# Kernel tuning notes

Hardware: AMD Instinct MI355X
Metric: run time of the kernel (lower is better)

The kernel has to match this reference:

```python
import jax, jax.numpy as jnp
import numpy as np

R_MAX = 32
S_MAX = 2
C_Z = 128
C_REL = 4 * R_MAX + 2 * S_MAX + 7 - 2 * R_MAX - 2 + 42  # 115
C_TOK = C_REL - (2 * R_MAX + 2) - (2 * S_MAX + 2) - 1    # 42


def setup_inputs() -> dict:
    key = jax.random.key(0)
    k0, k1, k2, k3, k4, k5 = jax.random.split(key, 6)
    B, N = 1, 1024
    asym_id = jax.random.randint(k0, (B, N), 0, 8)
    sym_id = jax.random.randint(k1, (B, N), 0, 8)
    entity_id = jax.random.randint(k2, (B, N), 0, 4)
    residue_index = jnp.sort(jax.random.randint(k3, (B, N), 0, 600), axis=-1)
    rel_tok_feat = jax.random.uniform(k4, (B, N, N, C_TOK), dtype=jnp.float32)
    W = jax.random.normal(k5, (C_REL, C_Z), dtype=jnp.float32) * 0.02
    return {
        "rel_tok_feat": rel_tok_feat,
        "W": W,
        "asym_id": asym_id,
        "sym_id": sym_id,
        "entity_id": entity_id,
        "residue_index": residue_index,
    }


def reference(rel_tok_feat, W, asym_id, sym_id, entity_id, residue_index):
    dt = rel_tok_feat.dtype
    # pairwise comparisons: [B, N, N]
    chain_same = asym_id[..., None] == asym_id[..., None, :]
    entity_same = entity_id[..., None] == entity_id[..., None, :]

    # relative residue offset, clipped, out-of-chain -> bin 2*r_max+1
    residue_offset = residue_index[..., None] - residue_index[..., None, :] + R_MAX
    clipped_res = jnp.clip(residue_offset, 0, 2 * R_MAX)
    d_res = jnp.where(chain_same, clipped_res, 2 * R_MAX + 1)
    rel_pos_feat = jax.nn.one_hot(d_res, 2 * R_MAX + 2, dtype=dt)  # [B,N,N,66]

    # relative chain offset
    chain_offset = sym_id[..., None] - sym_id[..., None, :] + S_MAX
    clipped_chain = jnp.clip(chain_offset, 0, 2 * S_MAX)
    d_chain = jnp.where(chain_same | (~entity_same), 2 * S_MAX + 1, clipped_chain)
    rel_chain_feat = jax.nn.one_hot(d_chain, 2 * S_MAX + 2, dtype=dt)  # [B,N,N,6]

    rel_feat = jnp.concatenate(
        [rel_pos_feat, rel_tok_feat, entity_same[..., None].astype(dt), rel_chain_feat],
        axis=-1,
    )  # [B,N,N,115]
    # Linear(c_rel_feat -> c_z, bias=False)
    return jnp.einsum("bijf,fc->bijc", rel_feat, W)
```

## Files before the change

kernel.cpp:

```cpp
#include <hip/hip_runtime.h>


typedef __attribute__((ext_vector_type(8))) short short8;
typedef __attribute__((ext_vector_type(4))) float floatx4;

#define NSEQ    1024
#define NTOK    42
#define CZ      128
#define CHUNK   64
#define NCHUNK  8
#define THREADS 256
#define TOK_DW  21
#define LDS_AW  36
#define NGROWS  73

__device__ __forceinline__ unsigned short f2bf(float f) {
    union { float f; unsigned int i; } v; v.f = f;
    unsigned int i = v.i;
    return (unsigned short)((i + 0x7fffu + ((i >> 16) & 1u)) >> 16);
}
__device__ __forceinline__ unsigned int packbf2(float x, float y) {
    return ((unsigned int)f2bf(y) << 16) | (unsigned int)f2bf(x);
}

__global__ __launch_bounds__(THREADS) void relpos_kernel(
    const float* __restrict__ tok,
    const float* __restrict__ W,
    const int* __restrict__ asym,
    const int* __restrict__ sym,
    const int* __restrict__ eid,
    const int* __restrict__ res,
    float* __restrict__ out)
{
    __shared__ __align__(16) unsigned int lds_Au[CHUNK * LDS_AW];
    __shared__ float lds_W[NGROWS * CZ];
    __shared__ int lds_flags[CHUNK];

    const int tid  = threadIdx.x;
    const int lane = tid & 63;
    const int wv   = tid >> 6;
    const int n    = lane & 15;
    const int q    = lane >> 4;

    for (int u = tid; u < NGROWS * CZ; u += THREADS) {
        int row = u >> 7;
        int wrow = row + (row >= 66 ? 42 : 0);
        lds_W[u] = W[wrow * CZ + (u & 127)];
    }

    short8 bfrag[2][8];
    #pragma unroll
    for (int ks = 0; ks < 2; ++ks) {
        #pragma unroll
        for (int nt = 0; nt < 8; ++nt) {
            short8 b;
            #pragma unroll
            for (int j = 0; j < 8; ++j) {
                int k = ks * 32 + q * 8 + j;
                b[j] = (k < NTOK) ? (short)f2bf(W[(66 + k) * CZ + nt * 16 + n]) : (short)0;
            }
            bfrag[ks][nt] = b;
        }
    }

    const int pblock = blockIdx.x * (CHUNK * NCHUNK);

    for (int ch = 0; ch < NCHUNK; ++ch) {
        const int p0 = pblock + ch * CHUNK;
        __syncthreads();

        const float2* tokv = (const float2*)tok + (size_t)p0 * TOK_DW;
        for (int u = tid; u < CHUNK * TOK_DW; u += THREADS) {
            float2 d = tokv[u];
            int pr = u / TOK_DW;
            int cu = u - pr * TOK_DW;
            lds_Au[pr * LDS_AW + cu] = packbf2(d.x, d.y);
        }
        for (int u = tid; u < CHUNK * 11; u += THREADS) {
            int pr = u / 11;
            lds_Au[pr * LDS_AW + 21 + (u - pr * 11)] = 0;
        }
        if (tid < CHUNK) {
            int p = p0 + tid;
            int i = p >> 10, j = p & (NSEQ - 1);
            bool cs = asym[i] == asym[j];
            bool es = eid[i] == eid[j];
            int ro = res[i] - res[j] + 32;
            ro = ro < 0 ? 0 : (ro > 64 ? 64 : ro);
            int dres = cs ? ro : 65;
            int co = sym[i] - sym[j] + 2;
            co = co < 0 ? 0 : (co > 4 ? 4 : co);
            int dch = (cs || !es) ? 5 : co;
            lds_flags[tid] = dres | (dch << 8) | ((es ? 1 : 0) << 16);
        }
        __syncthreads();

        const unsigned short* arow = (const unsigned short*)&lds_Au[(wv * 16 + n) * LDS_AW];
        short8 a0 = *(const short8*)(arow + q * 8);
        short8 a1 = *(const short8*)(arow + 32 + q * 8);
        floatx4 acc[8];
        #pragma unroll
        for (int nt = 0; nt < 8; ++nt) {
            floatx4 z = {0.f, 0.f, 0.f, 0.f};
            z = __builtin_amdgcn_mfma_f32_16x16x32_bf16(a0, bfrag[0][nt], z, 0, 0, 0);
            z = __builtin_amdgcn_mfma_f32_16x16x32_bf16(a1, bfrag[1][nt], z, 0, 0, 0);
            acc[nt] = z;
        }

        #pragma unroll
        for (int r = 0; r < 4; ++r) {
            int pl = wv * 16 + q * 4 + r;
            int fl = lds_flags[pl];
            const float* wres = lds_W + (fl & 0xff) * CZ;
            const float* wch  = lds_W + (67 + ((fl >> 8) & 0xff)) * CZ;
            float entf = (fl >> 16) ? 1.0f : 0.0f;
            const float* went = lds_W + 66 * CZ;
            size_t obase = ((size_t)(p0 + pl)) * CZ;
            #pragma unroll
            for (int nt = 0; nt < 8; ++nt) {
                int c = nt * 16 + n;
                out[obase + c] = acc[nt][r] + wres[c] + entf * went[c] + wch[c];
            }
        }
    }
}

extern "C" void kernel_launch(void* const* d_in, const int* in_sizes, int n_in,
                              void* d_out, int out_size, void* d_ws, size_t ws_size,
                              hipStream_t stream) {
    const float* tok = (const float*)d_in[0];
    const float* W   = (const float*)d_in[1];
    const int* asym  = (const int*)d_in[2];
    const int* sym   = (const int*)d_in[3];
    const int* eid   = (const int*)d_in[4];
    const int* res   = (const int*)d_in[5];
    float* out = (float*)d_out;

    const int npairs = NSEQ * NSEQ;
    const int grid = npairs / (CHUNK * NCHUNK);
    hipLaunchKernelGGL(relpos_kernel, dim3(grid), dim3(THREADS), 0, stream,
                       tok, W, asym, sym, eid, res, out);
}
```

Before: 775.9 us.

## Double-buffer token tiles with register prefetch and fold entity/chain one-hots into MFMA

Adds a two-slot LDS buffer and issues the next chunk's token and index loads into registers before the current MFMA and store phase, so global load latency overlaps compute and only one barrier per chunk remains. The entity-same and chain one-hot features are written as bf16 columns of the A tile (K grows from 42 to 49), which removes two LDS gathers and adds per output element. The W table is padded to reduce bank conflicts and an occupancy hint is added. The cost is more registers, a larger LDS footprint, and bf16 rounding of the extra W rows.

Result: faster. 699.0 us (-9.9%).

```diff
diff --git a/kernel.cpp b/kernel.cpp
--- a/kernel.cpp
+++ b/kernel.cpp
@@ -5,14 +5,15 @@
 typedef __attribute__((ext_vector_type(4))) float floatx4;
 
 #define NSEQ    1024
-#define NTOK    42
 #define CZ      128
 #define CHUNK   64
 #define NCHUNK  8
 #define THREADS 256
-#define TOK_DW  21
+#define KW      49
+#define TOKF2   21
 #define LDS_AW  36
-#define NGROWS  73
+#define WPAD    132
+#define NWROWS  66
 
 __device__ __forceinline__ unsigned short f2bf(float f) {
     union { float f; unsigned int i; } v; v.f = f;
@@ -23,7 +24,7 @@
     return ((unsigned int)f2bf(y) << 16) | (unsigned int)f2bf(x);
 }
 
-__global__ __launch_bounds__(THREADS) void relpos_kernel(
+__global__ __launch_bounds__(THREADS, 3) void relpos_kernel(
     const float* __restrict__ tok,
     const float* __restrict__ W,
     const int* __restrict__ asym,
@@ -32,9 +33,9 @@
     const int* __restrict__ res,
     float* __restrict__ out)
 {
-    __shared__ __align__(16) unsigned int lds_Au[CHUNK * LDS_AW];
-    __shared__ float lds_W[NGROWS * CZ];
-    __shared__ int lds_flags[CHUNK];
+    __shared__ __align__(16) unsigned int lds_Au[2 * CHUNK * LDS_AW];
+    __shared__ __align__(16) float lds_W[NWROWS * WPAD];
+    __shared__ int lds_flags[2 * CHUNK];
 
     const int tid  = threadIdx.x;
     const int lane = tid & 63;
@@ -42,11 +43,11 @@
     const int n    = lane & 15;
     const int q    = lane >> 4;
 
-    for (int u = tid; u < NGROWS * CZ; u += THREADS) {
-        int row = u >> 7;
-        int wrow = row + (row >= 66 ? 42 : 0);
-        lds_W[u] = W[wrow * CZ + (u & 127)];
+    for (int u4 = tid; u4 < NWROWS * (CZ / 4); u4 += THREADS) {
+        int row = u4 >> 5, c4 = (u4 & 31) << 2;
+        *(float4*)&lds_W[row * WPAD + c4] = *(const float4*)&W[row * CZ + c4];
     }
+    for (int u = tid; u < 2 * CHUNK * LDS_AW; u += THREADS) lds_Au[u] = 0u;
 
     short8 bfrag[2][8];
     #pragma unroll
@@ -57,45 +58,70 @@
             #pragma unroll
             for (int j = 0; j < 8; ++j) {
                 int k = ks * 32 + q * 8 + j;
-                b[j] = (k < NTOK) ? (short)f2bf(W[(66 + k) * CZ + nt * 16 + n]) : (short)0;
+                b[j] = (k < KW) ? (short)f2bf(W[(66 + k) * CZ + nt * 16 + n]) : (short)0;
             }
             bfrag[ks][nt] = b;
         }
     }
 
     const int pblock = blockIdx.x * (CHUNK * NCHUNK);
+    const bool fthr = (tid & 3) == 0;
+    const int  fpr  = tid >> 2;
+
+    __syncthreads();
+
+    {
+        const float2* tokv = (const float2*)tok + (size_t)pblock * TOKF2;
+        for (int u = tid; u < CHUNK * TOKF2; u += THREADS) {
+            float2 d = tokv[u];
+            lds_Au[(u / TOKF2) * LDS_AW + (u % TOKF2)] = packbf2(d.x, d.y);
+        }
+        if (fthr) {
+            int p = pblock + fpr;
+            int i = p >> 10, j = p & (NSEQ - 1);
+            int ai_ = asym[i], aj_ = asym[j], ei_ = eid[i], ej_ = eid[j];
+            int si_ = sym[i], sj_ = sym[j], ri_ = res[i], rj_ = res[j];
+            bool cs = ai_ == aj_, es = ei_ == ej_;
+            int ro = ri_ - rj_ + 32; ro = ro < 0 ? 0 : (ro > 64 ? 64 : ro);
+            int dres = cs ? ro : 65;
+            int co = si_ - sj_ + 2; co = co < 0 ? 0 : (co > 4 ? 4 : co);
+            int dch = (cs || !es) ? 5 : co;
+            const unsigned int one = 0x3F80u;
+            unsigned int* ar = lds_Au + fpr * LDS_AW;
+            ar[21] = (es ? one : 0u) | ((dch == 0 ? one : 0u) << 16);
+            ar[22] = (dch == 1 ? one : 0u) | ((dch == 2 ? one : 0u) << 16);
+            ar[23] = (dch == 3 ? one : 0u) | ((dch == 4 ? one : 0u) << 16);
+            ar[24] = (dch == 5 ? one : 0u);
+            lds_flags[fpr] = dres;
+        }
+    }
+    __syncthreads();
 
     for (int ch = 0; ch < NCHUNK; ++ch) {
+        const int par = ch & 1;
         const int p0 = pblock + ch * CHUNK;
-        __syncthreads();
+        const bool more = (ch + 1 < NCHUNK);
 
-        const float2* tokv = (const float2*)tok + (size_t)p0 * TOK_DW;
-        for (int u = tid; u < CHUNK * TOK_DW; u += THREADS) {
-            float2 d = tokv[u];
-            int pr = u / TOK_DW;
-            int cu = u - pr * TOK_DW;
-            lds_Au[pr * LDS_AW + cu] = packbf2(d.x, d.y);
+        float2 pf0, pf1, pf2, pf3, pf4, pf5;
+        int ai_, aj_, ei_, ej_, si_, sj_, ri_, rj_;
+        if (more) {
+            const float2* tokv = (const float2*)tok + (size_t)(p0 + CHUNK) * TOKF2;
+            pf0 = tokv[tid];
+            pf1 = tokv[tid + 256];
+            pf2 = tokv[tid + 512];
+            pf3 = tokv[tid + 768];
+            pf4 = tokv[tid + 1024];
+            if (tid < 64) pf5 = tokv[tid + 1280];
+            if (fthr) {
+                int p = p0 + CHUNK + fpr;
+                int i = p >> 10, j = p & (NSEQ - 1);
+                ai_ = asym[i]; aj_ = asym[j]; ei_ = eid[i]; ej_ = eid[j];
+                si_ = sym[i]; sj_ = sym[j]; ri_ = res[i]; rj_ = res[j];
+            }
         }
-        for (int u = tid; u < CHUNK * 11; u += THREADS) {
-            int pr = u / 11;
-            lds_Au[pr * LDS_AW + 21 + (u - pr * 11)] = 0;
-        }
-        if (tid < CHUNK) {
-            int p = p0 + tid;
-            int i = p >> 10, j = p & (NSEQ - 1);
-            bool cs = asym[i] == asym[j];
-            bool es = eid[i] == eid[j];
-            int ro = res[i] - res[j] + 32;
-            ro = ro < 0 ? 0 : (ro > 64 ? 64 : ro);
-            int dres = cs ? ro : 65;
-            int co = sym[i] - sym[j] + 2;
-            co = co < 0 ? 0 : (co > 4 ? 4 : co);
-            int dch = (cs || !es) ? 5 : co;
-            lds_flags[tid] = dres | (dch << 8) | ((es ? 1 : 0) << 16);
-        }
-        __syncthreads();
 
-        const unsigned short* arow = (const unsigned short*)&lds_Au[(wv * 16 + n) * LDS_AW];
+        const unsigned int* Abuf = lds_Au + par * (CHUNK * LDS_AW);
+        const unsigned short* arow = (const unsigned short*)(Abuf + (wv * 16 + n) * LDS_AW);
         short8 a0 = *(const short8*)(arow + q * 8);
         short8 a1 = *(const short8*)(arow + 32 + q * 8);
         floatx4 acc[8];
@@ -110,17 +136,44 @@
         #pragma unroll
         for (int r = 0; r < 4; ++r) {
             int pl = wv * 16 + q * 4 + r;
-            int fl = lds_flags[pl];
-            const float* wres = lds_W + (fl & 0xff) * CZ;
-            const float* wch  = lds_W + (67 + ((fl >> 8) & 0xff)) * CZ;
-            float entf = (fl >> 16) ? 1.0f : 0.0f;
-            const float* went = lds_W + 66 * CZ;
-            size_t obase = ((size_t)(p0 + pl)) * CZ;
+            int dres = lds_flags[par * CHUNK + pl];
+            const float* wres = lds_W + dres * WPAD;
+            size_t obase = (size_t)(p0 + pl) * CZ;
             #pragma unroll
             for (int nt = 0; nt < 8; ++nt) {
                 int c = nt * 16 + n;
-                out[obase + c] = acc[nt][r] + wres[c] + entf * went[c] + wch[c];
+                out[obase + c] = acc[nt][r] + wres[c];
             }
+        }
+
+        if (more) {
+            const int parn = par ^ 1;
+            unsigned int* Abn = lds_Au + parn * (CHUNK * LDS_AW);
+            int u;
+            u = tid;        Abn[(u / TOKF2) * LDS_AW + (u % TOKF2)] = packbf2(pf0.x, pf0.y);
+            u = tid + 256;  Abn[(u / TOKF2) * LDS_AW + (u % TOKF2)] = packbf2(pf1.x, pf1.y);
+            u = tid + 512;  Abn[(u / TOKF2) * LDS_AW + (u % TOKF2)] = packbf2(pf2.x, pf2.y);
+            u = tid + 768;  Abn[(u / TOKF2) * LDS_AW + (u % TOKF2)] = packbf2(pf3.x, pf3.y);
+            u = tid + 1024; Abn[(u / TOKF2) * LDS_AW + (u % TOKF2)] = packbf2(pf4.x, pf4.y);
+            if (tid < 64) {
+                u = tid + 1280;
+                Abn[(u / TOKF2) * LDS_AW + (u % TOKF2)] = packbf2(pf5.x, pf5.y);
+            }
+            if (fthr) {
+                bool cs = ai_ == aj_, es = ei_ == ej_;
+                int ro = ri_ - rj_ + 32; ro = ro < 0 ? 0 : (ro > 64 ? 64 : ro);
+                int dres = cs ? ro : 65;
+                int co = si_ - sj_ + 2; co = co < 0 ? 0 : (co > 4 ? 4 : co);
+                int dch = (cs || !es) ? 5 : co;
+                const unsigned int one = 0x3F80u;
+                unsigned int* ar = Abn + fpr * LDS_AW;
+                ar[21] = (es ? one : 0u) | ((dch == 0 ? one : 0u) << 16);
+                ar[22] = (dch == 1 ? one : 0u) | ((dch == 2 ? one : 0u) << 16);
+                ar[23] = (dch == 3 ? one : 0u) | ((dch == 4 ? one : 0u) << 16);
+                ar[24] = (dch == 5 ? one : 0u);
+                lds_flags[parn * CHUNK + fpr] = dres;
+            }
+            __syncthreads();
         }
     }
 }
```

## Build MFMA A-fragments in registers with prefetch, fold entity/chain one-hots into GEMM

Applied to the files above, without the earlier changes.

Drops the LDS staging of token features and per-pair flags. Each lane now loads its own token row directly into registers, prefetching the next chunk while the current one computes, and all per-chunk __syncthreads are removed. The entity and chain one-hot features are packed into the unused K slots of the second MFMA, so the epilogue adds only the residue-offset row from LDS (padded stride to cut bank conflicts). It also uses the hardware bf16 pack instruction and sets an occupancy hint of 3 blocks per CU. The costs are higher register pressure and less coalesced per-lane global loads of the token rows.

Result: faster. 683.6 us (-11.9%).

```diff
diff --git a/kernel.cpp b/kernel.cpp
--- a/kernel.cpp
+++ b/kernel.cpp
@@ -5,25 +5,28 @@
 typedef __attribute__((ext_vector_type(4))) float floatx4;
 
 #define NSEQ    1024
-#define NTOK    42
 #define CZ      128
 #define CHUNK   64
 #define NCHUNK  8
 #define THREADS 256
-#define TOK_DW  21
-#define LDS_AW  36
-#define NGROWS  73
+#define KW      49
+#define WROW    132
+#define NWROWS  66
 
-__device__ __forceinline__ unsigned short f2bf(float f) {
-    union { float f; unsigned int i; } v; v.f = f;
-    unsigned int i = v.i;
-    return (unsigned short)((i + 0x7fffu + ((i >> 16) & 1u)) >> 16);
-}
 __device__ __forceinline__ unsigned int packbf2(float x, float y) {
-    return ((unsigned int)f2bf(y) << 16) | (unsigned int)f2bf(x);
+    unsigned int r;
+    asm("v_cvt_pk_bf16_f32 %0, %1, %2" : "=v"(r) : "v"(x), "v"(y));
+    return r;
 }
 
-__global__ __launch_bounds__(THREADS) void relpos_kernel(
+struct Pref {
+    float2 t0, t1, t2, t3;
+    float2 t4, t5, t6, t7;
+    float2 t8;
+    int aj, sj, ej, rj;
+};
+
+__global__ __launch_bounds__(THREADS, 3) void relpos_kernel(
     const float* __restrict__ tok,
     const float* __restrict__ W,
     const int* __restrict__ asym,
@@ -32,9 +35,7 @@
     const int* __restrict__ res,
     float* __restrict__ out)
 {
-    __shared__ __align__(16) unsigned int lds_Au[CHUNK * LDS_AW];
-    __shared__ float lds_W[NGROWS * CZ];
-    __shared__ int lds_flags[CHUNK];
+    __shared__ __align__(16) float lds_W[NWROWS * WROW];
 
     const int tid  = threadIdx.x;
     const int lane = tid & 63;
@@ -42,10 +43,9 @@
     const int n    = lane & 15;
     const int q    = lane >> 4;
 
-    for (int u = tid; u < NGROWS * CZ; u += THREADS) {
-        int row = u >> 7;
-        int wrow = row + (row >= 66 ? 42 : 0);
-        lds_W[u] = W[wrow * CZ + (u & 127)];
+    for (int u4 = tid; u4 < NWROWS * 32; u4 += THREADS) {
+        int row = u4 >> 5, c4 = (u4 & 31) << 2;
+        *(float4*)&lds_W[row * WROW + c4] = *(const float4*)&W[row * CZ + c4];
     }
 
     short8 bfrag[2][8];
@@ -53,75 +53,104 @@
     for (int ks = 0; ks < 2; ++ks) {
         #pragma unroll
         for (int nt = 0; nt < 8; ++nt) {
-            short8 b;
+            unsigned int bu[4];
             #pragma unroll
-            for (int j = 0; j < 8; ++j) {
-                int k = ks * 32 + q * 8 + j;
-                b[j] = (k < NTOK) ? (short)f2bf(W[(66 + k) * CZ + nt * 16 + n]) : (short)0;
+            for (int j2 = 0; j2 < 4; ++j2) {
+                int k0 = ks * 32 + q * 8 + j2 * 2, k1 = k0 + 1;
+                float x = (k0 < KW) ? W[(66 + k0) * CZ + nt * 16 + n] : 0.f;
+                float y = (k1 < KW) ? W[(66 + k1) * CZ + nt * 16 + n] : 0.f;
+                bu[j2] = packbf2(x, y);
             }
-            bfrag[ks][nt] = b;
+            __builtin_memcpy(&bfrag[ks][nt], bu, 16);
         }
     }
 
     const int pblock = blockIdx.x * (CHUNK * NCHUNK);
+    const int irow = pblock >> 10;
+    const int ai = asym[irow], si = sym[irow], ei = eid[irow], ri = res[irow];
+    const int jb = (pblock & (NSEQ - 1)) + wv * 16 + n;
+
+    __syncthreads();
+
+    Pref cur, nxt;
+    {
+        const float2* base = (const float2*)(tok + (size_t)(pblock + wv * 16 + n) * 42);
+        cur.t0 = base[q * 4 + 0]; cur.t1 = base[q * 4 + 1];
+        cur.t2 = base[q * 4 + 2]; cur.t3 = base[q * 4 + 3];
+        float2 z = {0.f, 0.f};
+        cur.t4 = z; cur.t5 = z; cur.t6 = z; cur.t7 = z; cur.t8 = z;
+        if (q == 0) { cur.t4 = base[16]; cur.t5 = base[17]; cur.t6 = base[18]; cur.t7 = base[19]; }
+        if (q == 1) { cur.t8 = base[20]; }
+        cur.aj = asym[jb]; cur.sj = sym[jb]; cur.ej = eid[jb]; cur.rj = res[jb];
+    }
 
     for (int ch = 0; ch < NCHUNK; ++ch) {
         const int p0 = pblock + ch * CHUNK;
-        __syncthreads();
 
-        const float2* tokv = (const float2*)tok + (size_t)p0 * TOK_DW;
-        for (int u = tid; u < CHUNK * TOK_DW; u += THREADS) {
-            float2 d = tokv[u];
-            int pr = u / TOK_DW;
-            int cu = u - pr * TOK_DW;
-            lds_Au[pr * LDS_AW + cu] = packbf2(d.x, d.y);
+        bool cs = (ai == cur.aj), es = (ei == cur.ej);
+        int ro = ri - cur.rj + 32; ro = ro < 0 ? 0 : (ro > 64 ? 64 : ro);
+        int dres = cs ? ro : 65;
+        int co = si - cur.sj + 2; co = co < 0 ? 0 : (co > 4 ? 4 : co);
+        int dch = (cs || !es) ? 5 : co;
+        const unsigned int one = 0x3F80u;
+
+        unsigned int au[4], a1u[4];
+        au[0] = packbf2(cur.t0.x, cur.t0.y);
+        au[1] = packbf2(cur.t1.x, cur.t1.y);
+        au[2] = packbf2(cur.t2.x, cur.t2.y);
+        au[3] = packbf2(cur.t3.x, cur.t3.y);
+        if (q == 0) {
+            a1u[0] = packbf2(cur.t4.x, cur.t4.y);
+            a1u[1] = packbf2(cur.t5.x, cur.t5.y);
+            a1u[2] = packbf2(cur.t6.x, cur.t6.y);
+            a1u[3] = packbf2(cur.t7.x, cur.t7.y);
+        } else if (q == 1) {
+            a1u[0] = packbf2(cur.t8.x, cur.t8.y);
+            a1u[1] = (es ? one : 0u)        | ((dch == 0 ? one : 0u) << 16);
+            a1u[2] = (dch == 1 ? one : 0u)  | ((dch == 2 ? one : 0u) << 16);
+            a1u[3] = (dch == 3 ? one : 0u)  | ((dch == 4 ? one : 0u) << 16);
+        } else if (q == 2) {
+            a1u[0] = (dch == 5 ? one : 0u);
+            a1u[1] = 0u; a1u[2] = 0u; a1u[3] = 0u;
+        } else {
+            a1u[0] = 0u; a1u[1] = 0u; a1u[2] = 0u; a1u[3] = 0u;
         }
-        for (int u = tid; u < CHUNK * 11; u += THREADS) {
-            int pr = u / 11;
-            lds_Au[pr * LDS_AW + 21 + (u - pr * 11)] = 0;
+        short8 a0, a1;
+        __builtin_memcpy(&a0, au, 16);
+        __builtin_memcpy(&a1, a1u, 16);
+
+        if (ch + 1 < NCHUNK) {
+            const float2* base = (const float2*)(tok + (size_t)(p0 + CHUNK + wv * 16 + n) * 42);
+            nxt.t0 = base[q * 4 + 0]; nxt.t1 = base[q * 4 + 1];
+            nxt.t2 = base[q * 4 + 2]; nxt.t3 = base[q * 4 + 3];
+            float2 z = {0.f, 0.f};
+            nxt.t4 = z; nxt.t5 = z; nxt.t6 = z; nxt.t7 = z; nxt.t8 = z;
+            if (q == 0) { nxt.t4 = base[16]; nxt.t5 = base[17]; nxt.t6 = base[18]; nxt.t7 = base[19]; }
+            if (q == 1) { nxt.t8 = base[20]; }
+            int j = jb + (ch + 1) * CHUNK;
+            nxt.aj = asym[j]; nxt.sj = sym[j]; nxt.ej = eid[j]; nxt.rj = res[j];
         }
-        if (tid < CHUNK) {
-            int p = p0 + tid;
-            int i = p >> 10, j = p & (NSEQ - 1);
-            bool cs = asym[i] == asym[j];
-            bool es = eid[i] == eid[j];
-            int ro = res[i] - res[j] + 32;
-            ro = ro < 0 ? 0 : (ro > 64 ? 64 : ro);
-            int dres = cs ? ro : 65;
-            int co = sym[i] - sym[j] + 2;
-            co = co < 0 ? 0 : (co > 4 ? 4 : co);
-            int dch = (cs || !es) ? 5 : co;
-            lds_flags[tid] = dres | (dch << 8) | ((es ? 1 : 0) << 16);
-        }
-        __syncthreads();
 
-        const unsigned short* arow = (const unsigned short*)&lds_Au[(wv * 16 + n) * LDS_AW];
-        short8 a0 = *(const short8*)(arow + q * 8);
-        short8 a1 = *(const short8*)(arow + 32 + q * 8);
         floatx4 acc[8];
         #pragma unroll
         for (int nt = 0; nt < 8; ++nt) {
-            floatx4 z = {0.f, 0.f, 0.f, 0.f};
-            z = __builtin_amdgcn_mfma_f32_16x16x32_bf16(a0, bfrag[0][nt], z, 0, 0, 0);
-            z = __builtin_amdgcn_mfma_f32_16x16x32_bf16(a1, bfrag[1][nt], z, 0, 0, 0);
-            acc[nt] = z;
+            floatx4 z4 = {0.f, 0.f, 0.f, 0.f};
+            z4 = __builtin_amdgcn_mfma_f32_16x16x32_bf16(a0, bfrag[0][nt], z4, 0, 0, 0);
+            z4 = __builtin_amdgcn_mfma_f32_16x16x32_bf16(a1, bfrag[1][nt], z4, 0, 0, 0);
+            acc[nt] = z4;
         }
 
         #pragma unroll
         for (int r = 0; r < 4; ++r) {
-            int pl = wv * 16 + q * 4 + r;
-            int fl = lds_flags[pl];
-            const float* wres = lds_W + (fl & 0xff) * CZ;
-            const float* wch  = lds_W + (67 + ((fl >> 8) & 0xff)) * CZ;
-            float entf = (fl >> 16) ? 1.0f : 0.0f;
-            const float* went = lds_W + 66 * CZ;
-            size_t obase = ((size_t)(p0 + pl)) * CZ;
+            int dres_r = __shfl(dres, q * 4 + r, 64);
+            const float* wres = lds_W + dres_r * WROW + n;
+            float* op = out + (size_t)(p0 + wv * 16 + q * 4 + r) * CZ + n;
             #pragma unroll
-            for (int nt = 0; nt < 8; ++nt) {
-                int c = nt * 16 + n;
-                out[obase + c] = acc[nt][r] + wres[c] + entf * went[c] + wch[c];
-            }
+            for (int nt = 0; nt < 8; ++nt)
+                op[nt * 16] = acc[nt][r] + wres[nt * 16];
         }
+
+        if (ch + 1 < NCHUNK) cur = nxt;
     }
 }
 
```
